# Performance work log

Measured on AMD Instinct MI355X. Metric: run time of the kernel, lower is better.

The kernel has to match this reference:

```python
import jax, jax.numpy as jnp
import numpy as np

M, N, F = 512, 128, 512  # molecules, atoms per molecule, feature dim
HID, OUT = F // 4, 1


def setup_inputs() -> dict:
    key = jax.random.key(0)
    k1, k2, k3 = jax.random.split(key, 3)
    h = jax.random.normal(k1, (M, N, F), dtype=jnp.float32)
    W1 = jax.random.normal(k2, (F, HID), dtype=jnp.float32) * (1.0 / np.sqrt(F))
    b1 = jnp.zeros((HID,), dtype=jnp.float32)
    W2 = jax.random.normal(k3, (HID, OUT), dtype=jnp.float32) * (1.0 / np.sqrt(HID))
    b2 = jnp.zeros((OUT,), dtype=jnp.float32)
    return {"h": h, "W1": W1, "b1": b1, "W2": W2, "b2": b2}


def reference(h, W1, b1, W2, b2):
    # method == 'weighted_summation'
    # gate MLP: Linear -> ReLU -> Linear -> Sigmoid, per atom
    w = jax.nn.sigmoid(jax.nn.relu(h @ W1 + b1) @ W2 + b2)  # [M, N, OUT]
    # per-molecule weighted sum over atoms: mm(w_h.T, h) for each molecule,
    # concatenated along dim 0 -> [M*OUT, F] (OUT=1 -> [M, F])
    out = jnp.einsum('mno,mnf->mof', w, h)  # [M, OUT, F]
    return out.reshape(M * OUT, F)
```

## Files before the change

### kernel.cpp

```cpp
#include <hip/hip_runtime.h>
#include <hip/hip_bf16.h>


typedef unsigned short u16;
typedef unsigned int u32;
typedef __bf16 bf16x8 __attribute__((ext_vector_type(8)));
typedef float f32x4 __attribute__((ext_vector_type(4)));
typedef float f32x2 __attribute__((ext_vector_type(2)));
typedef u32 u32x4 __attribute__((ext_vector_type(4)));

#define M_MOL 512
#define N_ATOM 128
#define F_DIM 512
#define HID_DIM 128

static __device__ __forceinline__ u16 f2bf(float x) {
  u32 u = __float_as_uint(x);
  u32 r = (u + 0x7fffu + ((u >> 16) & 1u)) >> 16;
  return (u16)r;
}
static __device__ __forceinline__ bf16x8 load8bf(const u16* p) {
  u32x4 v = *(const u32x4*)p;
  return __builtin_bit_cast(bf16x8, v);
}
static __device__ __forceinline__ bf16x8 cvt8(const float* p) {
  u32x4 a = *(const u32x4*)p;
  u32x4 b = *(const u32x4*)(p + 4);
  u32x4 r;
  r[0] = (a[0] >> 16) | (a[1] & 0xffff0000u);
  r[1] = (a[2] >> 16) | (a[3] & 0xffff0000u);
  r[2] = (b[0] >> 16) | (b[1] & 0xffff0000u);
  r[3] = (b[2] >> 16) | (b[3] & 0xffff0000u);
  return __builtin_bit_cast(bf16x8, r);
}

__global__ __launch_bounds__(256) void transpose_w1(const float* __restrict__ W1,
                                                    u16* __restrict__ W1T) {
  __shared__ float tile[64][65];
  const int k0 = blockIdx.x * 64;
  const int n0 = blockIdx.y * 64;
  const int t = threadIdx.x;
  #pragma unroll
  for (int i = 0; i < 16; ++i) {
    const int lin = i * 256 + t;
    const int lr = lin >> 6, lc = lin & 63;
    tile[lc][lr] = W1[(size_t)(k0 + lr) * HID_DIM + (n0 + lc)];
  }
  __syncthreads();
  #pragma unroll
  for (int i = 0; i < 16; ++i) {
    const int lin = i * 256 + t;
    const int wr = lin >> 6, wc = lin & 63;
    W1T[(size_t)(n0 + wr) * F_DIM + (k0 + wc)] = f2bf(tile[wr][wc]);
  }
}

__global__ __launch_bounds__(256) void atom_pool_kernel(
    const float* __restrict__ h, const u16* __restrict__ W1T,
    const float* __restrict__ b1, const float* __restrict__ W2,
    const float* __restrict__ b2, float* __restrict__ out) {
  const int m = blockIdx.x;
  const int tid = threadIdx.x;
  const int wv = tid >> 6;
  const int lane = tid & 63;
  const int quad = lane >> 4;
  const int cl = lane & 15;

  __shared__ float w_s[N_ATOM];
  __shared__ float red[4][F_DIM];

  const float* hm = h + (size_t)m * N_ATOM * F_DIM;

  f32x4 acc[2][8];
  #pragma unroll
  for (int s = 0; s < 2; ++s)
    #pragma unroll
    for (int t = 0; t < 8; ++t)
      acc[s][t] = (f32x4){0.f, 0.f, 0.f, 0.f};

  const int strip0 = wv * 2;
  const float* arow0 = hm + (size_t)(strip0 * 16 + cl) * F_DIM;
  const float* arow1 = arow0 + 16 * F_DIM;
  const int kb = quad * 8;

  #pragma unroll 2
  for (int ks = 0; ks < 16; ++ks) {
    const int k = ks * 32 + kb;
    bf16x8 a0 = cvt8(arow0 + k);
    bf16x8 a1 = cvt8(arow1 + k);
    #pragma unroll
    for (int t = 0; t < 8; ++t) {
      bf16x8 bfr = load8bf(W1T + (size_t)(t * 16 + cl) * F_DIM + k);
      acc[0][t] = __builtin_amdgcn_mfma_f32_16x16x32_bf16(a0, bfr, acc[0][t], 0, 0, 0);
      acc[1][t] = __builtin_amdgcn_mfma_f32_16x16x32_bf16(a1, bfr, acc[1][t], 0, 0, 0);
    }
  }

  float psum[2][4] = {{0.f, 0.f, 0.f, 0.f}, {0.f, 0.f, 0.f, 0.f}};
  #pragma unroll
  for (int t = 0; t < 8; ++t) {
    const int hid = t * 16 + cl;
    const float b1v = b1[hid];
    const float w2v = W2[hid];
    #pragma unroll
    for (int s = 0; s < 2; ++s)
      #pragma unroll
      for (int r = 0; r < 4; ++r) {
        float tv = acc[s][t][r] + b1v;
        tv = fmaxf(tv, 0.f);
        psum[s][r] = fmaf(tv, w2v, psum[s][r]);
      }
  }
  #pragma unroll
  for (int off = 1; off < 16; off <<= 1) {
    #pragma unroll
    for (int s = 0; s < 2; ++s)
      #pragma unroll
      for (int r = 0; r < 4; ++r)
        psum[s][r] += __shfl_xor(psum[s][r], off, 64);
  }
  if (cl == 0) {
    const float b2v = b2[0];
    #pragma unroll
    for (int s = 0; s < 2; ++s)
      #pragma unroll
      for (int r = 0; r < 4; ++r) {
        const int atom = (strip0 + s) * 16 + quad * 4 + r;
        const float x = psum[s][r] + b2v;
        w_s[atom] = 1.f / (1.f + __expf(-x));
      }
  }
  __syncthreads();

  float facc[8] = {0.f, 0.f, 0.f, 0.f, 0.f, 0.f, 0.f, 0.f};
  const int f0 = lane * 8;
  const float* hrow = hm + (size_t)(wv * 32) * F_DIM + f0;
  #pragma unroll 4
  for (int i = 0; i < 32; ++i) {
    const float wn = w_s[wv * 32 + i];
    f32x4 h0 = *(const f32x4*)(hrow + (size_t)i * F_DIM);
    f32x4 h1 = *(const f32x4*)(hrow + (size_t)i * F_DIM + 4);
    #pragma unroll
    for (int j = 0; j < 4; ++j) {
      facc[j]     = fmaf(wn, h0[j], facc[j]);
      facc[j + 4] = fmaf(wn, h1[j], facc[j + 4]);
    }
  }
  #pragma unroll
  for (int j = 0; j < 8; ++j) red[wv][f0 + j] = facc[j];
  __syncthreads();

  {
    const int f = tid * 2;
    f32x2 o;
    o[0] = red[0][f] + red[1][f] + red[2][f] + red[3][f];
    o[1] = red[0][f + 1] + red[1][f + 1] + red[2][f + 1] + red[3][f + 1];
    *(f32x2*)(out + (size_t)m * F_DIM + f) = o;
  }
}

extern "C" void kernel_launch(void* const* d_in, const int* in_sizes, int n_in,
                              void* d_out, int out_size, void* d_ws, size_t ws_size,
                              hipStream_t stream) {
  const float* h  = (const float*)d_in[0];
  const float* W1 = (const float*)d_in[1];
  const float* b1 = (const float*)d_in[2];
  const float* W2 = (const float*)d_in[3];
  const float* b2 = (const float*)d_in[4];
  float* out = (float*)d_out;
  u16* W1T = (u16*)d_ws;

  transpose_w1<<<dim3(8, 2), 256, 0, stream>>>(W1, W1T);
  atom_pool_kernel<<<M_MOL, 256, 0, stream>>>(h, W1T, b1, W2, b2, out);
}
```

Measured before the change: 222.3 us.

## Use 8 waves per molecule with one atom strip each and prefetched A loads

The pooling kernel now runs 512 threads per block. Each of the 8 waves handles one 16-atom strip instead of two, so the block has more memory parallelism while the total work stays the same. The next k-step's h fragment is prefetched into registers before the MFMAs run, to hide load latency. The per-wave W1T fragment loads are repeated across twice as many waves, which adds L2 traffic, and the final reduction now sums 8 partial rows.

```diff
diff --git a/kernel.cpp b/kernel.cpp
--- a/kernel.cpp
+++ b/kernel.cpp
@@ -6,7 +6,6 @@
 typedef unsigned int u32;
 typedef __bf16 bf16x8 __attribute__((ext_vector_type(8)));
 typedef float f32x4 __attribute__((ext_vector_type(4)));
-typedef float f32x2 __attribute__((ext_vector_type(2)));
 typedef u32 u32x4 __attribute__((ext_vector_type(4)));
 
 #define M_MOL 512
@@ -23,9 +22,7 @@
   u32x4 v = *(const u32x4*)p;
   return __builtin_bit_cast(bf16x8, v);
 }
-static __device__ __forceinline__ bf16x8 cvt8(const float* p) {
-  u32x4 a = *(const u32x4*)p;
-  u32x4 b = *(const u32x4*)(p + 4);
+static __device__ __forceinline__ bf16x8 pack8(u32x4 a, u32x4 b) {
   u32x4 r;
   r[0] = (a[0] >> 16) | (a[1] & 0xffff0000u);
   r[1] = (a[2] >> 16) | (a[3] & 0xffff0000u);
@@ -55,7 +52,7 @@
   }
 }
 
-__global__ __launch_bounds__(256) void atom_pool_kernel(
+__global__ __launch_bounds__(512, 4) void atom_pool_kernel(
     const float* __restrict__ h, const u16* __restrict__ W1T,
     const float* __restrict__ b1, const float* __restrict__ W2,
     const float* __restrict__ b2, float* __restrict__ out) {
@@ -67,77 +64,67 @@
   const int cl = lane & 15;
 
   __shared__ float w_s[N_ATOM];
-  __shared__ float red[4][F_DIM];
+  __shared__ float red[8][F_DIM];
 
   const float* hm = h + (size_t)m * N_ATOM * F_DIM;
 
-  f32x4 acc[2][8];
+  f32x4 acc[8];
   #pragma unroll
-  for (int s = 0; s < 2; ++s)
-    #pragma unroll
-    for (int t = 0; t < 8; ++t)
-      acc[s][t] = (f32x4){0.f, 0.f, 0.f, 0.f};
+  for (int t = 0; t < 8; ++t) acc[t] = (f32x4){0.f, 0.f, 0.f, 0.f};
 
-  const int strip0 = wv * 2;
-  const float* arow0 = hm + (size_t)(strip0 * 16 + cl) * F_DIM;
-  const float* arow1 = arow0 + 16 * F_DIM;
+  const float* arow = hm + (size_t)(wv * 16 + cl) * F_DIM;
   const int kb = quad * 8;
 
+  u32x4 a_lo = *(const u32x4*)(arow + kb);
+  u32x4 a_hi = *(const u32x4*)(arow + kb + 4);
   #pragma unroll 2
   for (int ks = 0; ks < 16; ++ks) {
     const int k = ks * 32 + kb;
-    bf16x8 a0 = cvt8(arow0 + k);
-    bf16x8 a1 = cvt8(arow1 + k);
+    bf16x8 afr = pack8(a_lo, a_hi);
+    if (ks < 15) {
+      a_lo = *(const u32x4*)(arow + k + 32);
+      a_hi = *(const u32x4*)(arow + k + 36);
+    }
     #pragma unroll
     for (int t = 0; t < 8; ++t) {
       bf16x8 bfr = load8bf(W1T + (size_t)(t * 16 + cl) * F_DIM + k);
-      acc[0][t] = __builtin_amdgcn_mfma_f32_16x16x32_bf16(a0, bfr, acc[0][t], 0, 0, 0);
-      acc[1][t] = __builtin_amdgcn_mfma_f32_16x16x32_bf16(a1, bfr, acc[1][t], 0, 0, 0);
+      acc[t] = __builtin_amdgcn_mfma_f32_16x16x32_bf16(afr, bfr, acc[t], 0, 0, 0);
     }
   }
 
-  float psum[2][4] = {{0.f, 0.f, 0.f, 0.f}, {0.f, 0.f, 0.f, 0.f}};
+  float psum[4] = {0.f, 0.f, 0.f, 0.f};
   #pragma unroll
   for (int t = 0; t < 8; ++t) {
     const int hid = t * 16 + cl;
     const float b1v = b1[hid];
     const float w2v = W2[hid];
     #pragma unroll
-    for (int s = 0; s < 2; ++s)
-      #pragma unroll
-      for (int r = 0; r < 4; ++r) {
-        float tv = acc[s][t][r] + b1v;
-        tv = fmaxf(tv, 0.f);
-        psum[s][r] = fmaf(tv, w2v, psum[s][r]);
-      }
+    for (int r = 0; r < 4; ++r) {
+      float tv = fmaxf(acc[t][r] + b1v, 0.f);
+      psum[r] = fmaf(tv, w2v, psum[r]);
+    }
   }
   #pragma unroll
-  for (int off = 1; off < 16; off <<= 1) {
+  for (int off = 1; off < 16; off <<= 1)
     #pragma unroll
-    for (int s = 0; s < 2; ++s)
-      #pragma unroll
-      for (int r = 0; r < 4; ++r)
-        psum[s][r] += __shfl_xor(psum[s][r], off, 64);
-  }
+    for (int r = 0; r < 4; ++r)
+      psum[r] += __shfl_xor(psum[r], off, 64);
   if (cl == 0) {
     const float b2v = b2[0];
     #pragma unroll
-    for (int s = 0; s < 2; ++s)
-      #pragma unroll
-      for (int r = 0; r < 4; ++r) {
-        const int atom = (strip0 + s) * 16 + quad * 4 + r;
-        const float x = psum[s][r] + b2v;
-        w_s[atom] = 1.f / (1.f + __expf(-x));
-      }
+    for (int r = 0; r < 4; ++r) {
+      const int atom = wv * 16 + quad * 4 + r;
+      w_s[atom] = 1.f / (1.f + __expf(-(psum[r] + b2v)));
+    }
   }
   __syncthreads();
 
   float facc[8] = {0.f, 0.f, 0.f, 0.f, 0.f, 0.f, 0.f, 0.f};
   const int f0 = lane * 8;
-  const float* hrow = hm + (size_t)(wv * 32) * F_DIM + f0;
+  const float* hrow = hm + (size_t)(wv * 16) * F_DIM + f0;
   #pragma unroll 4
-  for (int i = 0; i < 32; ++i) {
-    const float wn = w_s[wv * 32 + i];
+  for (int i = 0; i < 16; ++i) {
+    const float wn = w_s[wv * 16 + i];
     f32x4 h0 = *(const f32x4*)(hrow + (size_t)i * F_DIM);
     f32x4 h1 = *(const f32x4*)(hrow + (size_t)i * F_DIM + 4);
     #pragma unroll
@@ -151,11 +138,11 @@
   __syncthreads();
 
   {
-    const int f = tid * 2;
-    f32x2 o;
-    o[0] = red[0][f] + red[1][f] + red[2][f] + red[3][f];
-    o[1] = red[0][f + 1] + red[1][f + 1] + red[2][f + 1] + red[3][f + 1];
-    *(f32x2*)(out + (size_t)m * F_DIM + f) = o;
+    const int f = tid;
+    float o = 0.f;
+    #pragma unroll
+    for (int k = 0; k < 8; ++k) o += red[k][f];
+    out[(size_t)m * F_DIM + f] = o;
   }
 }
 
@@ -171,5 +158,5 @@
   u16* W1T = (u16*)d_ws;
 
   transpose_w1<<<dim3(8, 2), 256, 0, stream>>>(W1, W1T);
-  atom_pool_kernel<<<M_MOL, 256, 0, stream>>>(h, W1T, b1, W2, b2, out);
+  atom_pool_kernel<<<M_MOL, 512, 0, stream>>>(h, W1T, b1, W2, b2, out);
 }
```

New measurement: 249.5 us. 12.2% more time.
